# Performance work log

Hardware: AMD Instinct MI355X
Metric: run time of the kernel (lower is better)

Reference implementation:

```python
import jax, jax.numpy as jnp
import numpy as np

A, D, H, NACT = 8, 128, 64, 16  # n_agents, input_shape, rnn_hidden_dim, n_actions
B = 16384


def setup_inputs() -> dict:
    key = jax.random.key(0)
    ks = jax.random.split(key, 12)
    s = 1.0 / np.sqrt(H)
    si = 1.0 / np.sqrt(D)
    inp = {
        'inputs': jax.random.normal(ks[0], (B * A, D), dtype=jnp.float32),
        'hidden_state': jax.random.normal(ks[1], (B, A, H), dtype=jnp.float32),
        # stacked per-agent (non-shared) weights, PyTorch default-init scale
        'W1': jax.random.uniform(ks[2], (A, H, D), jnp.float32, -si, si),
        'b1': jax.random.uniform(ks[3], (A, H), jnp.float32, -si, si),
        'W_ih': jax.random.uniform(ks[4], (A, 3 * H, H), jnp.float32, -s, s),
        'b_ih': jax.random.uniform(ks[5], (A, 3 * H), jnp.float32, -s, s),
        'W_hh': jax.random.uniform(ks[6], (A, 3 * H, H), jnp.float32, -s, s),
        'b_hh': jax.random.uniform(ks[7], (A, 3 * H), jnp.float32, -s, s),
        'W2': jax.random.uniform(ks[8], (A, NACT, H), jnp.float32, -s, s),
        'b2': jax.random.uniform(ks[9], (A, NACT), jnp.float32, -s, s),
    }
    return inp


def reference(inputs, hidden_state, W1, b1, W_ih, b_ih, W_hh, b_hh, W2, b2):
    x = inputs.reshape(-1, A, D)                 # [B, A, D]
    h = hidden_state.reshape(-1, A, H)           # [B, A, H]
    # fc1 + ReLU, batched over agents
    z1 = jax.nn.relu(jnp.einsum('bad,ahd->bah', x, W1) + b1)
    # GRUCell (PyTorch convention: gates r, z, n)
    gi = jnp.einsum('bah,agh->bag', z1, W_ih) + b_ih   # [B, A, 3H]
    gh = jnp.einsum('bah,agh->bag', h, W_hh) + b_hh
    i_r, i_z, i_n = jnp.split(gi, 3, axis=-1)
    h_r, h_z, h_n = jnp.split(gh, 3, axis=-1)
    r = jax.nn.sigmoid(i_r + h_r)
    z = jax.nn.sigmoid(i_z + h_z)
    n = jnp.tanh(i_n + r * h_n)
    h_new = (1.0 - z) * n + z * h                # [B, A, H]
    # fc2
    q = jnp.einsum('bah,anh->ban', h_new, W2) + b2   # [B, A, NACT]
    # match torch: cat(qs, dim=-1).view(-1, n_actions) == reshape [B*A, NACT]
    return q.reshape(-1, NACT), h_new
```

## Files before the change

### kernel.cpp

```cpp
#include <hip/hip_runtime.h>
#include <hip/hip_bf16.h>
#include <cstddef>

#define NAGENT 8
#define DIN    128
#define HID    64
#define NACT   16

typedef __attribute__((ext_vector_type(8))) short bf16x8;
typedef __attribute__((ext_vector_type(4))) float f32x4;

__device__ __forceinline__ short f2bf(float f) {
    __hip_bfloat16 h = __float2bfloat16(f);
    union { __hip_bfloat16 h; short s; } u; u.h = h;
    return u.s;
}
__device__ __forceinline__ float sigmoid_f(float v) { return 1.0f / (1.0f + __expf(-v)); }
__device__ __forceinline__ float tanh_f(float v) {
    v = fminf(fmaxf(v, -15.0f), 15.0f);
    float e = __expf(2.0f * v);
    return (e - 1.0f) / (e + 1.0f);
}
__device__ __forceinline__ bf16x8 cvt8pair(float4 v0, float4 v1) {
    bf16x8 r;
    r[0] = f2bf(v0.x); r[1] = f2bf(v0.y); r[2] = f2bf(v0.z); r[3] = f2bf(v0.w);
    r[4] = f2bf(v1.x); r[5] = f2bf(v1.y); r[6] = f2bf(v1.z); r[7] = f2bf(v1.w);
    return r;
}

extern "C" __global__ void __launch_bounds__(256)
conv_weights_packed(const float* __restrict__ W1, const float* __restrict__ Wih,
                    const float* __restrict__ Whh, const float* __restrict__ W2,
                    short* __restrict__ ws)
{
    const int a = blockIdx.y;
    const int c = blockIdx.x * 256 + threadIdx.x;
    if (c >= 4224) return;
    const int lane = c & 63, lr = lane & 15, lk = lane >> 4;
    const float* src;
    if (c < 1024) {
        int n = c >> 8, k = (c >> 6) & 3;
        src = W1 + a * 8192 + (n * 16 + lr) * 128 + k * 32 + lk * 8;
    } else if (c < 2560) {
        int idx = (c - 1024) >> 6;
        int g = idx >> 3, n = (idx >> 1) & 3, kk = idx & 1;
        src = Wih + a * 12288 + (g * 64 + n * 16 + lr) * 64 + kk * 32 + lk * 8;
    } else if (c < 4096) {
        int idx = (c - 2560) >> 6;
        int g = idx >> 3, n = (idx >> 1) & 3, kk = idx & 1;
        src = Whh + a * 12288 + (g * 64 + n * 16 + lr) * 64 + kk * 32 + lk * 8;
    } else {
        int kk = (c - 4096) >> 6;
        src = W2 + a * 1024 + lr * 64 + kk * 32 + lk * 8;
    }
    float4 v0 = ((const float4*)src)[0];
    float4 v1 = ((const float4*)src)[1];
    bf16x8 o = cvt8pair(v0, v1);
    *(bf16x8*)(ws + (size_t)a * 33792 + (size_t)c * 8) = o;
}

extern "C" __global__ void __launch_bounds__(256, 4)
rnn_main(const float* __restrict__ x,
         const float* __restrict__ hin,
         const float* __restrict__ b1, const float* __restrict__ bih,
         const float* __restrict__ bhh, const float* __restrict__ b2,
         const short* __restrict__ wsp,
         float* __restrict__ qout,
         float* __restrict__ hout)
{
    const int a    = blockIdx.y;
    const int t    = threadIdx.x;
    const int wid  = t >> 6;
    const int lane = t & 63;
    const int lr   = lane & 15;
    const int lk   = lane >> 4;

    __shared__ short zs[4 * 1024];
    char* zb = (char*)(zs + wid * 1024);

    const short* wsA = wsp + (size_t)a * 33792;
    const int tile = blockIdx.x * 4 + wid;
    const int arow = tile * 16 + lr;

    const float* xrow = x + ((size_t)arow * NAGENT + a) * DIN + lk * 8;
    const float* hrow = hin + ((size_t)arow * NAGENT + a) * HID + lk * 8;
    bf16x8 hf0 = cvt8pair(*(const float4*)(hrow),      *(const float4*)(hrow + 4));
    bf16x8 hf1 = cvt8pair(*(const float4*)(hrow + 32), *(const float4*)(hrow + 36));

    {
        f32x4 acc1[4];
        #pragma unroll
        for (int n = 0; n < 4; ++n) {
            float bv = b1[a * HID + n * 16 + lr];
            acc1[n] = (f32x4){bv, bv, bv, bv};
        }
        #pragma unroll
        for (int k = 0; k < 4; ++k) {
            bf16x8 xk = cvt8pair(*(const float4*)(xrow + k * 32),
                                 *(const float4*)(xrow + k * 32 + 4));
            #pragma unroll
            for (int n = 0; n < 4; ++n) {
                bf16x8 wb = *(const bf16x8*)(wsA + ((n * 4 + k) * 64 + lane) * 8);
                acc1[n] = __builtin_amdgcn_mfma_f32_16x16x32_bf16(xk, wb, acc1[n], 0, 0, 0);
            }
        }
        #pragma unroll
        for (int n = 0; n < 4; ++n)
            #pragma unroll
            for (int j = 0; j < 4; ++j) {
                int row = lk * 4 + j, col = n * 16 + lr;
                *(short*)(zb + row * 128 + ((col * 2) ^ ((row & 7) << 4))) =
                    f2bf(fmaxf(acc1[n][j], 0.0f));
            }
    }

    bf16x8 za0 = *(const bf16x8*)(zb + lr * 128 + ((0 * 64 + lk * 16) ^ ((lr & 7) << 4)));
    bf16x8 za1 = *(const bf16x8*)(zb + lr * 128 + ((1 * 64 + lk * 16) ^ ((lr & 7) << 4)));

    #pragma unroll 1
    for (int n = 0; n < 4; ++n) {
        float bhr = bhh[a * 192 +   0 + n * 16 + lr];
        float bhz = bhh[a * 192 +  64 + n * 16 + lr];
        float bhn = bhh[a * 192 + 128 + n * 16 + lr];
        f32x4 aHr = (f32x4){bhr, bhr, bhr, bhr};
        f32x4 aHz = (f32x4){bhz, bhz, bhz, bhz};
        f32x4 aHn = (f32x4){bhn, bhn, bhn, bhn};
        #pragma unroll
        for (int kk = 0; kk < 2; ++kk) {
            bf16x8 hfk = kk ? hf1 : hf0;
            bf16x8 whr = *(const bf16x8*)(wsA + 20480 + (((0 * 4 + n) * 2 + kk) * 64 + lane) * 8);
            bf16x8 whz = *(const bf16x8*)(wsA + 20480 + (((1 * 4 + n) * 2 + kk) * 64 + lane) * 8);
            bf16x8 whn = *(const bf16x8*)(wsA + 20480 + (((2 * 4 + n) * 2 + kk) * 64 + lane) * 8);
            aHr = __builtin_amdgcn_mfma_f32_16x16x32_bf16(hfk, whr, aHr, 0, 0, 0);
            aHz = __builtin_amdgcn_mfma_f32_16x16x32_bf16(hfk, whz, aHz, 0, 0, 0);
            aHn = __builtin_amdgcn_mfma_f32_16x16x32_bf16(hfk, whn, aHn, 0, 0, 0);
        }

        float bir = bih[a * 192 +   0 + n * 16 + lr];
        float biz = bih[a * 192 +  64 + n * 16 + lr];
        float bin_ = bih[a * 192 + 128 + n * 16 + lr];
        f32x4 aIr = (f32x4){bir, bir, bir, bir};
        f32x4 aIz = (f32x4){biz, biz, biz, biz};
        f32x4 aIn = (f32x4){bin_, bin_, bin_, bin_};
        #pragma unroll
        for (int kk = 0; kk < 2; ++kk) {
            bf16x8 zak = kk ? za1 : za0;
            bf16x8 wir = *(const bf16x8*)(wsA + 8192 + (((0 * 4 + n) * 2 + kk) * 64 + lane) * 8);
            bf16x8 wiz = *(const bf16x8*)(wsA + 8192 + (((1 * 4 + n) * 2 + kk) * 64 + lane) * 8);
            bf16x8 win = *(const bf16x8*)(wsA + 8192 + (((2 * 4 + n) * 2 + kk) * 64 + lane) * 8);
            aIr = __builtin_amdgcn_mfma_f32_16x16x32_bf16(zak, wir, aIr, 0, 0, 0);
            aIz = __builtin_amdgcn_mfma_f32_16x16x32_bf16(zak, wiz, aIz, 0, 0, 0);
            aIn = __builtin_amdgcn_mfma_f32_16x16x32_bf16(zak, win, aIn, 0, 0, 0);
        }

        #pragma unroll
        for (int j = 0; j < 4; ++j) {
            int row = lk * 4 + j, col = n * 16 + lr;
            float hp = hin[((size_t)(tile * 16 + row) * NAGENT + a) * HID + col];
            float r  = sigmoid_f(aIr[j] + aHr[j]);
            float zv = sigmoid_f(aIz[j] + aHz[j]);
            float nn = tanh_f(aIn[j] + r * aHn[j]);
            float hv = (1.0f - zv) * nn + zv * hp;
            hout[((size_t)(tile * 16 + row) * NAGENT + a) * HID + col] = hv;
            *(short*)(zb + row * 128 + ((col * 2) ^ ((row & 7) << 4))) = f2bf(hv);
        }
    }

    {
        float bq = b2[a * NACT + lr];
        f32x4 q = (f32x4){bq, bq, bq, bq};
        bf16x8 ha0 = *(const bf16x8*)(zb + lr * 128 + ((0 * 64 + lk * 16) ^ ((lr & 7) << 4)));
        bf16x8 ha1 = *(const bf16x8*)(zb + lr * 128 + ((1 * 64 + lk * 16) ^ ((lr & 7) << 4)));
        bf16x8 w2f0 = *(const bf16x8*)(wsA + 32768 + (0 * 64 + lane) * 8);
        bf16x8 w2f1 = *(const bf16x8*)(wsA + 32768 + (1 * 64 + lane) * 8);
        q = __builtin_amdgcn_mfma_f32_16x16x32_bf16(ha0, w2f0, q, 0, 0, 0);
        q = __builtin_amdgcn_mfma_f32_16x16x32_bf16(ha1, w2f1, q, 0, 0, 0);
        #pragma unroll
        for (int j = 0; j < 4; ++j)
            qout[((size_t)(tile * 16 + lk * 4 + j) * NAGENT + a) * NACT + lr] = q[j];
    }
}

extern "C" void kernel_launch(void* const* d_in, const int* in_sizes, int n_in,
                              void* d_out, int out_size, void* d_ws, size_t ws_size,
                              hipStream_t stream)
{
    const float* x   = (const float*)d_in[0];
    const float* hin = (const float*)d_in[1];
    const float* W1  = (const float*)d_in[2];
    const float* b1  = (const float*)d_in[3];
    const float* Wih = (const float*)d_in[4];
    const float* bih = (const float*)d_in[5];
    const float* Whh = (const float*)d_in[6];
    const float* bhh = (const float*)d_in[7];
    const float* W2  = (const float*)d_in[8];
    const float* b2  = (const float*)d_in[9];

    const int B = in_sizes[0] / (NAGENT * DIN);

    float* qout = (float*)d_out;
    float* hout = (float*)d_out + (size_t)B * NAGENT * NACT;

    short* wsp = (short*)d_ws;

    conv_weights_packed<<<dim3(17, NAGENT), 256, 0, stream>>>(W1, Wih, Whh, W2, wsp);

    dim3 grid(B / 64, NAGENT);
    rnn_main<<<grid, 256, 0, stream>>>(x, hin, b1, bih, bhh, b2, wsp, qout, hout);
}
```

Measured before the change: 48.52 us.

## Process two 16-row tiles per wave to reuse weight fragments

Each wave now handles two 16-row batch tiles instead of one, so every weight fragment loaded from the packed workspace feeds two MFMAs. The grid is halved and the launch bound drops to 2 blocks/SM to make room for the extra accumulators and registers. This trades lower occupancy and fewer blocks for half the weight-load traffic per row and more independent MFMAs in flight.

```diff
diff --git a/kernel.cpp b/kernel.cpp
--- a/kernel.cpp
+++ b/kernel.cpp
@@ -59,7 +59,7 @@
     *(bf16x8*)(ws + (size_t)a * 33792 + (size_t)c * 8) = o;
 }
 
-extern "C" __global__ void __launch_bounds__(256, 4)
+extern "C" __global__ void __launch_bounds__(256, 2)
 rnn_main(const float* __restrict__ x,
          const float* __restrict__ hin,
          const float* __restrict__ b1, const float* __restrict__ bih,
@@ -75,33 +75,45 @@
     const int lr   = lane & 15;
     const int lk   = lane >> 4;
 
-    __shared__ short zs[4 * 1024];
-    char* zb = (char*)(zs + wid * 1024);
+    __shared__ short zs[8 * 1024];
+    char* zbA = (char*)(zs + (wid * 2 + 0) * 1024);
+    char* zbB = (char*)(zs + (wid * 2 + 1) * 1024);
 
     const short* wsA = wsp + (size_t)a * 33792;
-    const int tile = blockIdx.x * 4 + wid;
-    const int arow = tile * 16 + lr;
-
-    const float* xrow = x + ((size_t)arow * NAGENT + a) * DIN + lk * 8;
-    const float* hrow = hin + ((size_t)arow * NAGENT + a) * HID + lk * 8;
-    bf16x8 hf0 = cvt8pair(*(const float4*)(hrow),      *(const float4*)(hrow + 4));
-    bf16x8 hf1 = cvt8pair(*(const float4*)(hrow + 32), *(const float4*)(hrow + 36));
+    const int tileA = blockIdx.x * 8 + wid * 2;
+    const int tileB = tileA + 1;
+    const int arowA = tileA * 16 + lr;
+    const int arowB = tileB * 16 + lr;
+
+    const float* xrowA = x + ((size_t)arowA * NAGENT + a) * DIN + lk * 8;
+    const float* xrowB = x + ((size_t)arowB * NAGENT + a) * DIN + lk * 8;
+    const float* hrowA = hin + ((size_t)arowA * NAGENT + a) * HID + lk * 8;
+    const float* hrowB = hin + ((size_t)arowB * NAGENT + a) * HID + lk * 8;
+
+    bf16x8 hfA0 = cvt8pair(*(const float4*)(hrowA),      *(const float4*)(hrowA + 4));
+    bf16x8 hfA1 = cvt8pair(*(const float4*)(hrowA + 32), *(const float4*)(hrowA + 36));
+    bf16x8 hfB0 = cvt8pair(*(const float4*)(hrowB),      *(const float4*)(hrowB + 4));
+    bf16x8 hfB1 = cvt8pair(*(const float4*)(hrowB + 32), *(const float4*)(hrowB + 36));
 
     {
-        f32x4 acc1[4];
+        f32x4 accA[4], accB[4];
         #pragma unroll
         for (int n = 0; n < 4; ++n) {
             float bv = b1[a * HID + n * 16 + lr];
-            acc1[n] = (f32x4){bv, bv, bv, bv};
+            accA[n] = (f32x4){bv, bv, bv, bv};
+            accB[n] = accA[n];
         }
         #pragma unroll
         for (int k = 0; k < 4; ++k) {
-            bf16x8 xk = cvt8pair(*(const float4*)(xrow + k * 32),
-                                 *(const float4*)(xrow + k * 32 + 4));
+            bf16x8 xkA = cvt8pair(*(const float4*)(xrowA + k * 32),
+                                  *(const float4*)(xrowA + k * 32 + 4));
+            bf16x8 xkB = cvt8pair(*(const float4*)(xrowB + k * 32),
+                                  *(const float4*)(xrowB + k * 32 + 4));
             #pragma unroll
             for (int n = 0; n < 4; ++n) {
                 bf16x8 wb = *(const bf16x8*)(wsA + ((n * 4 + k) * 64 + lane) * 8);
-                acc1[n] = __builtin_amdgcn_mfma_f32_16x16x32_bf16(xk, wb, acc1[n], 0, 0, 0);
+                accA[n] = __builtin_amdgcn_mfma_f32_16x16x32_bf16(xkA, wb, accA[n], 0, 0, 0);
+                accB[n] = __builtin_amdgcn_mfma_f32_16x16x32_bf16(xkB, wb, accB[n], 0, 0, 0);
             }
         }
         #pragma unroll
@@ -109,75 +121,108 @@
             #pragma unroll
             for (int j = 0; j < 4; ++j) {
                 int row = lk * 4 + j, col = n * 16 + lr;
-                *(short*)(zb + row * 128 + ((col * 2) ^ ((row & 7) << 4))) =
-                    f2bf(fmaxf(acc1[n][j], 0.0f));
-            }
-    }
-
-    bf16x8 za0 = *(const bf16x8*)(zb + lr * 128 + ((0 * 64 + lk * 16) ^ ((lr & 7) << 4)));
-    bf16x8 za1 = *(const bf16x8*)(zb + lr * 128 + ((1 * 64 + lk * 16) ^ ((lr & 7) << 4)));
+                int off = row * 128 + ((col * 2) ^ ((row & 7) << 4));
+                *(short*)(zbA + off) = f2bf(fmaxf(accA[n][j], 0.0f));
+                *(short*)(zbB + off) = f2bf(fmaxf(accB[n][j], 0.0f));
+            }
+    }
+
+    bf16x8 zaA0 = *(const bf16x8*)(zbA + lr * 128 + ((0 * 64 + lk * 16) ^ ((lr & 7) << 4)));
+    bf16x8 zaA1 = *(const bf16x8*)(zbA + lr * 128 + ((1 * 64 + lk * 16) ^ ((lr & 7) << 4)));
+    bf16x8 zaB0 = *(const bf16x8*)(zbB + lr * 128 + ((0 * 64 + lk * 16) ^ ((lr & 7) << 4)));
+    bf16x8 zaB1 = *(const bf16x8*)(zbB + lr * 128 + ((1 * 64 + lk * 16) ^ ((lr & 7) << 4)));
 
     #pragma unroll 1
     for (int n = 0; n < 4; ++n) {
         float bhr = bhh[a * 192 +   0 + n * 16 + lr];
         float bhz = bhh[a * 192 +  64 + n * 16 + lr];
         float bhn = bhh[a * 192 + 128 + n * 16 + lr];
-        f32x4 aHr = (f32x4){bhr, bhr, bhr, bhr};
-        f32x4 aHz = (f32x4){bhz, bhz, bhz, bhz};
-        f32x4 aHn = (f32x4){bhn, bhn, bhn, bhn};
+        f32x4 aHrA = (f32x4){bhr, bhr, bhr, bhr}, aHrB = aHrA;
+        f32x4 aHzA = (f32x4){bhz, bhz, bhz, bhz}, aHzB = aHzA;
+        f32x4 aHnA = (f32x4){bhn, bhn, bhn, bhn}, aHnB = aHnA;
         #pragma unroll
         for (int kk = 0; kk < 2; ++kk) {
-            bf16x8 hfk = kk ? hf1 : hf0;
+            bf16x8 hfAk = kk ? hfA1 : hfA0;
+            bf16x8 hfBk = kk ? hfB1 : hfB0;
             bf16x8 whr = *(const bf16x8*)(wsA + 20480 + (((0 * 4 + n) * 2 + kk) * 64 + lane) * 8);
             bf16x8 whz = *(const bf16x8*)(wsA + 20480 + (((1 * 4 + n) * 2 + kk) * 64 + lane) * 8);
             bf16x8 whn = *(const bf16x8*)(wsA + 20480 + (((2 * 4 + n) * 2 + kk) * 64 + lane) * 8);
-            aHr = __builtin_amdgcn_mfma_f32_16x16x32_bf16(hfk, whr, aHr, 0, 0, 0);
-            aHz = __builtin_amdgcn_mfma_f32_16x16x32_bf16(hfk, whz, aHz, 0, 0, 0);
-            aHn = __builtin_amdgcn_mfma_f32_16x16x32_bf16(hfk, whn, aHn, 0, 0, 0);
-        }
-
-        float bir = bih[a * 192 +   0 + n * 16 + lr];
-        float biz = bih[a * 192 +  64 + n * 16 + lr];
-        float bin_ = bih[a * 192 + 128 + n * 16 + lr];
-        f32x4 aIr = (f32x4){bir, bir, bir, bir};
-        f32x4 aIz = (f32x4){biz, biz, biz, biz};
-        f32x4 aIn = (f32x4){bin_, bin_, bin_, bin_};
+            aHrA = __builtin_amdgcn_mfma_f32_16x16x32_bf16(hfAk, whr, aHrA, 0, 0, 0);
+            aHrB = __builtin_amdgcn_mfma_f32_16x16x32_bf16(hfBk, whr, aHrB, 0, 0, 0);
+            aHzA = __builtin_amdgcn_mfma_f32_16x16x32_bf16(hfAk, whz, aHzA, 0, 0, 0);
+            aHzB = __builtin_amdgcn_mfma_f32_16x16x32_bf16(hfBk, whz, aHzB, 0, 0, 0);
+            aHnA = __builtin_amdgcn_mfma_f32_16x16x32_bf16(hfAk, whn, aHnA, 0, 0, 0);
+            aHnB = __builtin_amdgcn_mfma_f32_16x16x32_bf16(hfBk, whn, aHnB, 0, 0, 0);
+        }
+
+        f32x4 aIrA, aIrB, aIzA, aIzB, aInA, aInB;
+        {
+            float bir  = bih[a * 192 +   0 + n * 16 + lr];
+            float biz  = bih[a * 192 +  64 + n * 16 + lr];
+            float bin_ = bih[a * 192 + 128 + n * 16 + lr];
+            aIrA = (f32x4){bir, bir, bir, bir};   aIrB = aIrA;
+            aIzA = (f32x4){biz, biz, biz, biz};   aIzB = aIzA;
+            aInA = (f32x4){bin_, bin_, bin_, bin_}; aInB = aInA;
+        }
         #pragma unroll
         for (int kk = 0; kk < 2; ++kk) {
-            bf16x8 zak = kk ? za1 : za0;
+            bf16x8 zaAk = kk ? zaA1 : zaA0;
+            bf16x8 zaBk = kk ? zaB1 : zaB0;
             bf16x8 wir = *(const bf16x8*)(wsA + 8192 + (((0 * 4 + n) * 2 + kk) * 64 + lane) * 8);
             bf16x8 wiz = *(const bf16x8*)(wsA + 8192 + (((1 * 4 + n) * 2 + kk) * 64 + lane) * 8);
             bf16x8 win = *(const bf16x8*)(wsA + 8192 + (((2 * 4 + n) * 2 + kk) * 64 + lane) * 8);
-            aIr = __builtin_amdgcn_mfma_f32_16x16x32_bf16(zak, wir, aIr, 0, 0, 0);
-            aIz = __builtin_amdgcn_mfma_f32_16x16x32_bf16(zak, wiz, aIz, 0, 0, 0);
-            aIn = __builtin_amdgcn_mfma_f32_16x16x32_bf16(zak, win, aIn, 0, 0, 0);
+            aIrA = __builtin_amdgcn_mfma_f32_16x16x32_bf16(zaAk, wir, aIrA, 0, 0, 0);
+            aIrB = __builtin_amdgcn_mfma_f32_16x16x32_bf16(zaBk, wir, aIrB, 0, 0, 0);
+            aIzA = __builtin_amdgcn_mfma_f32_16x16x32_bf16(zaAk, wiz, aIzA, 0, 0, 0);
+            aIzB = __builtin_amdgcn_mfma_f32_16x16x32_bf16(zaBk, wiz, aIzB, 0, 0, 0);
+            aInA = __builtin_amdgcn_mfma_f32_16x16x32_bf16(zaAk, win, aInA, 0, 0, 0);
+            aInB = __builtin_amdgcn_mfma_f32_16x16x32_bf16(zaBk, win, aInB, 0, 0, 0);
         }
 
         #pragma unroll
         for (int j = 0; j < 4; ++j) {
             int row = lk * 4 + j, col = n * 16 + lr;
-            float hp = hin[((size_t)(tile * 16 + row) * NAGENT + a) * HID + col];
-            float r  = sigmoid_f(aIr[j] + aHr[j]);
-            float zv = sigmoid_f(aIz[j] + aHz[j]);
-            float nn = tanh_f(aIn[j] + r * aHn[j]);
-            float hv = (1.0f - zv) * nn + zv * hp;
-            hout[((size_t)(tile * 16 + row) * NAGENT + a) * HID + col] = hv;
-            *(short*)(zb + row * 128 + ((col * 2) ^ ((row & 7) << 4))) = f2bf(hv);
+            int off = row * 128 + ((col * 2) ^ ((row & 7) << 4));
+            {
+                float hp = hin[((size_t)(tileA * 16 + row) * NAGENT + a) * HID + col];
+                float r  = sigmoid_f(aIrA[j] + aHrA[j]);
+                float zv = sigmoid_f(aIzA[j] + aHzA[j]);
+                float nn = tanh_f(aInA[j] + r * aHnA[j]);
+                float hv = (1.0f - zv) * nn + zv * hp;
+                hout[((size_t)(tileA * 16 + row) * NAGENT + a) * HID + col] = hv;
+                *(short*)(zbA + off) = f2bf(hv);
+            }
+            {
+                float hp = hin[((size_t)(tileB * 16 + row) * NAGENT + a) * HID + col];
+                float r  = sigmoid_f(aIrB[j] + aHrB[j]);
+                float zv = sigmoid_f(aIzB[j] + aHzB[j]);
+                float nn = tanh_f(aInB[j] + r * aHnB[j]);
+                float hv = (1.0f - zv) * nn + zv * hp;
+                hout[((size_t)(tileB * 16 + row) * NAGENT + a) * HID + col] = hv;
+                *(short*)(zbB + off) = f2bf(hv);
+            }
         }
     }
 
     {
         float bq = b2[a * NACT + lr];
-        f32x4 q = (f32x4){bq, bq, bq, bq};
-        bf16x8 ha0 = *(const bf16x8*)(zb + lr * 128 + ((0 * 64 + lk * 16) ^ ((lr & 7) << 4)));
-        bf16x8 ha1 = *(const bf16x8*)(zb + lr * 128 + ((1 * 64 + lk * 16) ^ ((lr & 7) << 4)));
+        f32x4 qA = (f32x4){bq, bq, bq, bq};
+        f32x4 qB = qA;
         bf16x8 w2f0 = *(const bf16x8*)(wsA + 32768 + (0 * 64 + lane) * 8);
         bf16x8 w2f1 = *(const bf16x8*)(wsA + 32768 + (1 * 64 + lane) * 8);
-        q = __builtin_amdgcn_mfma_f32_16x16x32_bf16(ha0, w2f0, q, 0, 0, 0);
-        q = __builtin_amdgcn_mfma_f32_16x16x32_bf16(ha1, w2f1, q, 0, 0, 0);
-        #pragma unroll
-        for (int j = 0; j < 4; ++j)
-            qout[((size_t)(tile * 16 + lk * 4 + j) * NAGENT + a) * NACT + lr] = q[j];
+        bf16x8 haA0 = *(const bf16x8*)(zbA + lr * 128 + ((0 * 64 + lk * 16) ^ ((lr & 7) << 4)));
+        bf16x8 haA1 = *(const bf16x8*)(zbA + lr * 128 + ((1 * 64 + lk * 16) ^ ((lr & 7) << 4)));
+        bf16x8 haB0 = *(const bf16x8*)(zbB + lr * 128 + ((0 * 64 + lk * 16) ^ ((lr & 7) << 4)));
+        bf16x8 haB1 = *(const bf16x8*)(zbB + lr * 128 + ((1 * 64 + lk * 16) ^ ((lr & 7) << 4)));
+        qA = __builtin_amdgcn_mfma_f32_16x16x32_bf16(haA0, w2f0, qA, 0, 0, 0);
+        qB = __builtin_amdgcn_mfma_f32_16x16x32_bf16(haB0, w2f0, qB, 0, 0, 0);
+        qA = __builtin_amdgcn_mfma_f32_16x16x32_bf16(haA1, w2f1, qA, 0, 0, 0);
+        qB = __builtin_amdgcn_mfma_f32_16x16x32_bf16(haB1, w2f1, qB, 0, 0, 0);
+        #pragma unroll
+        for (int j = 0; j < 4; ++j) {
+            qout[((size_t)(tileA * 16 + lk * 4 + j) * NAGENT + a) * NACT + lr] = qA[j];
+            qout[((size_t)(tileB * 16 + lk * 4 + j) * NAGENT + a) * NACT + lr] = qB[j];
+        }
     }
 }
 
@@ -205,6 +250,6 @@
 
     conv_weights_packed<<<dim3(17, NAGENT), 256, 0, stream>>>(W1, Wih, Whh, W2, wsp);
 
-    dim3 grid(B / 64, NAGENT);
+    dim3 grid(B / 128, NAGENT);
     rnn_main<<<grid, 256, 0, stream>>>(x, hin, b1, bih, bhh, b2, wsp, qout, hout);
 }
```

New measurement: 58.88 us. +21.3%, slower.
